# Kernel tuning notes

Hardware: AMD Instinct MI355X
Metric: run time of the kernel (lower is better)

## Reference

```python
import jax, jax.numpy as jnp
import numpy as np

N_HEAD = 16


def setup_inputs() -> dict:
    key = jax.random.key(0)
    ks = jax.random.split(key, 3)
    B, T, C = 4, 2048, 1024
    x = jax.random.normal(ks[0], (B, T, C), dtype=jnp.float32)
    w_attn = jax.random.normal(ks[1], (3 * C, C), dtype=jnp.float32) * (1.0 / np.sqrt(C))
    b_attn = jnp.zeros((3 * C,), dtype=jnp.float32)
    w_proj = jax.random.normal(ks[2], (C, C), dtype=jnp.float32) * (1.0 / np.sqrt(C))
    b_proj = jnp.zeros((C,), dtype=jnp.float32)
    return {"x": x, "w_attn": w_attn, "b_attn": b_attn, "w_proj": w_proj, "b_proj": b_proj}


def reference(x, w_attn, b_attn, w_proj, b_proj):
    B, T, C = x.shape
    H = N_HEAD
    D = C // H
    qkv = x @ w_attn.T + b_attn                      # [B, T, 3C]
    q, k, v = jnp.split(qkv, 3, axis=-1)
    # [B, T, C] -> [B, H, T, D]
    q = q.reshape(B, T, H, D).transpose(0, 2, 1, 3)
    k = k.reshape(B, T, H, D).transpose(0, 2, 1, 3)
    v = v.reshape(B, T, H, D).transpose(0, 2, 1, 3)
    scale = 1.0 / np.sqrt(D).astype(np.float32)
    att = jnp.einsum('bhqd,bhkd->bhqk', q, k) * scale  # [B, H, T, T]
    causal = jnp.tril(jnp.ones((T, T), dtype=bool))
    att = jnp.where(causal[None, None], att, -jnp.inf)
    att = jax.nn.softmax(att, axis=-1)
    y = jnp.einsum('bhqk,bhkd->bhqd', att, v)          # [B, H, T, D]
    y = y.transpose(0, 2, 1, 3).reshape(B, T, C)
    return y @ w_proj.T + b_proj
```

## Files before the change

### kernel.cpp

```cpp
#include <hip/hip_runtime.h>
#include <hip/hip_bf16.h>
#include <stdint.h>

typedef __attribute__((ext_vector_type(8))) short bf16x8;
typedef __attribute__((ext_vector_type(4))) float f32x4;

#define MFMA16(a, b, c) __builtin_amdgcn_mfma_f32_16x16x32_bf16((a), (b), (c), 0, 0, 0)

__device__ __forceinline__ unsigned short f2bf(float f) {
  unsigned int u = __builtin_bit_cast(unsigned int, f);
  unsigned int r = (u + 0x7fffu + ((u >> 16) & 1u)) >> 16;
  return (unsigned short)r;
}

__device__ __forceinline__ void gload16(const unsigned short* g, unsigned short* lds_dst) {
  __builtin_amdgcn_global_load_lds(
      (const __attribute__((address_space(1))) unsigned int*)g,
      (__attribute__((address_space(3))) unsigned int*)lds_dst, 16, 0, 0);
}

__global__ void cvt_f32_bf16(const float* __restrict__ in, unsigned short* __restrict__ out, long n) {
  long i = ((long)blockIdx.x * blockDim.x + threadIdx.x) * 4;
  long stride = (long)gridDim.x * blockDim.x * 4;
  for (; i < n; i += stride) {
    float4 v = *(const float4*)(in + i);
    ushort4 o;
    o.x = f2bf(v.x); o.y = f2bf(v.y); o.z = f2bf(v.z); o.w = f2bf(v.w);
    *(ushort4*)(out + i) = o;
  }
}

template <int EPI, int NB>
__global__ __launch_bounds__(512, 2)
void gemm_bt(const unsigned short* __restrict__ A,
             const unsigned short* __restrict__ Bt,
             const float* __restrict__ bias,
             int M, int N, int K,
             unsigned short* __restrict__ q_out,
             unsigned short* __restrict__ k_out,
             unsigned short* __restrict__ vt_out,
             float* __restrict__ f_out) {
  constexpr int BNT = NB * 64;
  alignas(16) __shared__ unsigned short Alds[2][2][128 * 64];
  alignas(16) __shared__ unsigned short Blds[2][BNT * 64];
  const int t = threadIdx.x, w = t >> 6, l = t & 63;
  const int bm = blockIdx.x, bn = blockIdx.y;
  const int wm = w >> 2, wn = w & 3;
  const int lo = l & 15, hi = l >> 4, swk = lo & 7;

  f32x4 acc[8][NB];
  const f32x4 zero = {0.f, 0.f, 0.f, 0.f};
#pragma unroll
  for (int i = 0; i < 8; ++i)
#pragma unroll
    for (int j = 0; j < NB; ++j) acc[i][j] = zero;

  const int sr = t >> 3;
  const int gsrcE = ((t & 7) ^ (sr & 7)) * 8;
  const unsigned short* Asrc = A + (long)(bm * 256 + sr) * K + gsrcE;
  const unsigned short* Bsrc = Bt + (long)(bn * BNT + sr) * K + gsrcE;

#define STAGE_AH(sb, qh, koff) do {                                    \
    unsigned short* d_ = &Alds[sb][qh][w * 512];                       \
    const unsigned short* s_ = Asrc + (long)(qh) * 64 * K + (koff);    \
    gload16(s_, d_); gload16(s_ + 128L * K, d_ + 4096); } while (0)
#define STAGE_B(sb, koff) do {                                         \
    _Pragma("unroll")                                                  \
    for (int c_ = 0; c_ < NB; ++c_)                                    \
      gload16(Bsrc + (long)c_ * 64 * K + (koff),                       \
              &Blds[sb][c_ * 4096 + w * 512]); } while (0)

  STAGE_AH(0, 0, 0);
  STAGE_B(0, 0);
  STAGE_AH(0, 1, 0);
  asm volatile("s_waitcnt vmcnt(2)" ::: "memory");
  __builtin_amdgcn_sched_barrier(0);
  __builtin_amdgcn_s_barrier();

  const int lrA = (wm * 64 + lo) * 64;
  const int lrB = (wn * (NB * 16) + lo) * 64;
  const int gk0 = ((hi) ^ swk) * 8;
  const int gk1 = ((4 + hi) ^ swk) * 8;

  bf16x8 af[4][2], blo[2][2], bhi[2];

  for (int kt = 0; kt < 16; ++kt) {
    const int c = kt & 1, nb = c ^ 1;
    const bool st = (kt < 15);
    const int koff = (kt + 1) * 64;
    const unsigned short* A0 = Alds[c][0];
    const unsigned short* A1 = Alds[c][1];
    const unsigned short* Bs = Blds[c];

#pragma unroll
    for (int ii = 0; ii < 4; ++ii) {
      af[ii][0] = *(const bf16x8*)&A0[lrA + ii * 1024 + gk0];
      af[ii][1] = *(const bf16x8*)&A0[lrA + ii * 1024 + gk1];
    }
#pragma unroll
    for (int jj = 0; jj < NB - 1; ++jj) {
      blo[jj][0] = *(const bf16x8*)&Bs[lrB + jj * 1024 + gk0];
      blo[jj][1] = *(const bf16x8*)&Bs[lrB + jj * 1024 + gk1];
    }
    if (st) STAGE_AH(nb, 0, koff);
    __builtin_amdgcn_s_barrier();
    asm volatile("s_waitcnt lgkmcnt(0)" ::: "memory");
    __builtin_amdgcn_sched_barrier(0);
    __builtin_amdgcn_s_setprio(1);
#pragma unroll
    for (int ii = 0; ii < 4; ++ii)
#pragma unroll
      for (int jj = 0; jj < NB - 1; ++jj) {
        acc[ii][jj] = MFMA16(af[ii][0], blo[jj][0], acc[ii][jj]);
        acc[ii][jj] = MFMA16(af[ii][1], blo[jj][1], acc[ii][jj]);
      }
    __builtin_amdgcn_s_setprio(0);
    __builtin_amdgcn_s_barrier();

    bhi[0] = *(const bf16x8*)&Bs[lrB + (NB - 1) * 1024 + gk0];
    bhi[1] = *(const bf16x8*)&Bs[lrB + (NB - 1) * 1024 + gk1];
    if (st) STAGE_B(nb, koff);
    __builtin_amdgcn_s_barrier();
    asm volatile("s_waitcnt lgkmcnt(0)" ::: "memory");
    __builtin_amdgcn_sched_barrier(0);
    __builtin_amdgcn_s_setprio(1);
#pragma unroll
    for (int ii = 0; ii < 4; ++ii) {
      acc[ii][NB - 1] = MFMA16(af[ii][0], bhi[0], acc[ii][NB - 1]);
      acc[ii][NB - 1] = MFMA16(af[ii][1], bhi[1], acc[ii][NB - 1]);
    }
    __builtin_amdgcn_s_setprio(0);
    if (st) {
      if constexpr (NB == 3) { asm volatile("s_waitcnt vmcnt(5)" ::: "memory"); }
      else                   { asm volatile("s_waitcnt vmcnt(4)" ::: "memory"); }
    } else {
      asm volatile("s_waitcnt vmcnt(0)" ::: "memory");
    }
    __builtin_amdgcn_sched_barrier(0);
    __builtin_amdgcn_s_barrier();

#pragma unroll
    for (int ii = 0; ii < 4; ++ii) {
      af[ii][0] = *(const bf16x8*)&A1[lrA + ii * 1024 + gk0];
      af[ii][1] = *(const bf16x8*)&A1[lrA + ii * 1024 + gk1];
    }
    if (st) STAGE_AH(nb, 1, koff);
    __builtin_amdgcn_s_barrier();
    asm volatile("s_waitcnt lgkmcnt(0)" ::: "memory");
    __builtin_amdgcn_sched_barrier(0);
    __builtin_amdgcn_s_setprio(1);
#pragma unroll
    for (int ii = 0; ii < 4; ++ii) {
      acc[4 + ii][NB - 1] = MFMA16(af[ii][0], bhi[0], acc[4 + ii][NB - 1]);
      acc[4 + ii][NB - 1] = MFMA16(af[ii][1], bhi[1], acc[4 + ii][NB - 1]);
    }
    __builtin_amdgcn_s_setprio(0);
    __builtin_amdgcn_s_barrier();

    __builtin_amdgcn_s_setprio(1);
#pragma unroll
    for (int ii = 0; ii < 4; ++ii)
#pragma unroll
      for (int jj = 0; jj < NB - 1; ++jj) {
        acc[4 + ii][jj] = MFMA16(af[ii][0], blo[jj][0], acc[4 + ii][jj]);
        acc[4 + ii][jj] = MFMA16(af[ii][1], blo[jj][1], acc[4 + ii][jj]);
      }
    __builtin_amdgcn_s_setprio(0);
    if (st) {
      asm volatile("s_waitcnt vmcnt(2)" ::: "memory");
      __builtin_amdgcn_sched_barrier(0);
    }
    __builtin_amdgcn_s_barrier();
  }
#undef STAGE_AH
#undef STAGE_B

#pragma unroll
  for (int i = 0; i < 8; ++i) {
#pragma unroll
    for (int j = 0; j < NB; ++j) {
#pragma unroll
      for (int r = 0; r < 4; ++r) {
        int row = bm * 256 + wm * 128 + i * 16 + hi * 4 + r;
        int col = bn * BNT + wn * (NB * 16) + j * 16 + lo;
        float v = acc[i][j][r] + bias[col];
        if (EPI == 0) {
          int b = row >> 11, tt = row & 2047;
          int seg = col >> 10, cc = col & 1023;
          int h = cc >> 6, d = cc & 63;
          long bh = (long)(b * 16 + h);
          if (seg == 0)      q_out[(bh * 2048 + tt) * 64 + d] = f2bf(v * 0.1803368801111f);
          else if (seg == 1) k_out[(bh * 2048 + tt) * 64 + d] = f2bf(v);
          else               vt_out[(bh * 64 + d) * 2048 + tt] = f2bf(v);
        } else {
          f_out[(long)row * N + col] = v;
        }
      }
    }
  }
}

__global__ __launch_bounds__(512, 4)
void attn_kernel(const unsigned short* __restrict__ Q,
                 const unsigned short* __restrict__ K,
                 const unsigned short* __restrict__ Vt,
                 unsigned short* __restrict__ Y) {
  alignas(16) __shared__ unsigned short Kbuf[2][64 * 64];
  alignas(16) __shared__ unsigned short Vbuf[2][64 * 64];
  alignas(16) __shared__ unsigned short pbuf[8][16 * 64];
  const int t = threadIdx.x, w = t >> 6, l = t & 63;
  const int lo = l & 15, hi = l >> 4;
  const int bh = blockIdx.x;
  const int p = blockIdx.y;
  const int b = bh >> 4, h = bh & 15;
  const int sA = p, sB = 15 - p;
  const int nA = 2 * p + 2;
  const int nTot = 34;
  const unsigned short* Qp = Q + (long)bh * 2048 * 64;
  const unsigned short* Kp = K + (long)bh * 2048 * 64;
  const unsigned short* Vp = Vt + (long)bh * 64 * 2048;
  unsigned short* pw = pbuf[w];

  const short one_bf = (short)0x3F80;
  const bf16x8 ones = {one_bf, one_bf, one_bf, one_bf, one_bf, one_bf, one_bf, one_bf};
  const f32x4 zero = {0.f, 0.f, 0.f, 0.f};

  const int qbA = sA * 128 + w * 16;
  const int qbB = sB * 128 + w * 16;

  bf16x8 qf0, qf1;
  f32x4 lsum;
  f32x4 oacc[4];

  qf0 = *(const bf16x8*)&Qp[(qbA + lo) * 64 + hi * 8];
  qf1 = *(const bf16x8*)&Qp[(qbA + lo) * 64 + 32 + hi * 8];
  lsum = zero;
#pragma unroll
  for (int dg = 0; dg < 4; ++dg) oacc[dg] = zero;

  const int srow = t >> 3;
  const int scw = ((t & 7) ^ (srow & 7)) * 8;
  const int sw = lo & 7;

#define STAGE(kvoff, bufidx)                                          \
  do {                                                                \
    unsigned short* KB_ = Kbuf[bufidx] + w * 512;                     \
    unsigned short* VB_ = Vbuf[bufidx] + w * 512;                     \
    gload16(Kp + (long)((kvoff) + srow) * 64 + scw, KB_);             \
    gload16(Vp + (long)srow * 2048 + (kvoff) + scw, VB_);             \
  } while (0)

  STAGE(0, 0);
  __syncthreads();

  for (int g = 0; g < nTot; ++g) {
    const bool inA = (g < nA);
    const int kvb = (inA ? g : g - nA) * 64;
    const int cur = g & 1;
    if (g + 1 < nTot) {
      const int jn = (g + 1 < nA) ? g + 1 : g + 1 - nA;
      STAGE(jn * 64, cur ^ 1);
    }
    const int qbase = inA ? qbA : qbB;
    if (kvb <= qbase + 15) {
      const unsigned short* KB = Kbuf[cur];
      const unsigned short* VB = Vbuf[cur];
      f32x4 s[4];
#pragma unroll
      for (int cg = 0; cg < 4; ++cg) s[cg] = zero;
      __builtin_amdgcn_s_setprio(1);
#pragma unroll
      for (int cg = 0; cg < 4; ++cg) {
        bf16x8 k0 = *(const bf16x8*)&KB[(cg * 16 + lo) * 64 + ((hi) ^ sw) * 8];
        bf16x8 k1 = *(const bf16x8*)&KB[(cg * 16 + lo) * 64 + ((4 + hi) ^ sw) * 8];
        s[cg] = MFMA16(k0, qf0, s[cg]);
        s[cg] = MFMA16(k1, qf1, s[cg]);
      }
      __builtin_amdgcn_s_setprio(0);
      if (kvb + 63 > qbase) {
        const int limit = qbase + lo - kvb;
#pragma unroll
        for (int cg = 0; cg < 4; ++cg)
#pragma unroll
          for (int r = 0; r < 4; ++r)
            if (cg * 16 + hi * 4 + r > limit) s[cg][r] = -__builtin_inff();
      }
#pragma unroll
      for (int cg = 0; cg < 4; ++cg) {
        float p0 = exp2f(s[cg][0]);
        float p1 = exp2f(s[cg][1]);
        float p2 = exp2f(s[cg][2]);
        float p3 = exp2f(s[cg][3]);
        unsigned int u0, u1;
        asm("v_cvt_pk_bf16_f32 %0, %1, %2" : "=v"(u0) : "v"(p0), "v"(p1));
        asm("v_cvt_pk_bf16_f32 %0, %1, %2" : "=v"(u1) : "v"(p2), "v"(p3));
        const int gg = (cg * 2 + (hi >> 1)) ^ sw;
        uint2 val; val.x = u0; val.y = u1;
        *(uint2*)&pw[lo * 64 + gg * 8 + (hi & 1) * 4] = val;
      }
      asm volatile("s_waitcnt lgkmcnt(0)" ::: "memory");
      bf16x8 pa0 = *(const bf16x8*)&pw[lo * 64 + ((hi) ^ sw) * 8];
      bf16x8 pa1 = *(const bf16x8*)&pw[lo * 64 + ((4 + hi) ^ sw) * 8];
      __builtin_amdgcn_s_setprio(1);
      lsum = MFMA16(pa0, ones, lsum);
      lsum = MFMA16(pa1, ones, lsum);
#pragma unroll
      for (int dg = 0; dg < 4; ++dg) {
        bf16x8 vv0 = *(const bf16x8*)&VB[(dg * 16 + lo) * 64 + ((hi) ^ sw) * 8];
        bf16x8 vv1 = *(const bf16x8*)&VB[(dg * 16 + lo) * 64 + ((4 + hi) ^ sw) * 8];
        oacc[dg] = MFMA16(pa0, vv0, oacc[dg]);
        oacc[dg] = MFMA16(pa1, vv1, oacc[dg]);
      }
      __builtin_amdgcn_s_setprio(0);
    }
    if (g == nA - 1) {
#pragma unroll
      for (int r = 0; r < 4; ++r) {
        float inv = 1.0f / lsum[r];
        int rowg = qbA + hi * 4 + r;
        long base = ((long)b * 2048 + rowg) * 1024 + h * 64;
#pragma unroll
        for (int dg = 0; dg < 4; ++dg)
          Y[base + dg * 16 + lo] = f2bf(oacc[dg][r] * inv);
      }
      qf0 = *(const bf16x8*)&Qp[(qbB + lo) * 64 + hi * 8];
      qf1 = *(const bf16x8*)&Qp[(qbB + lo) * 64 + 32 + hi * 8];
      lsum = zero;
#pragma unroll
      for (int dg = 0; dg < 4; ++dg) oacc[dg] = zero;
    }
    __syncthreads();
  }

#pragma unroll
  for (int r = 0; r < 4; ++r) {
    float inv = 1.0f / lsum[r];
    int rowg = qbB + hi * 4 + r;
    long base = ((long)b * 2048 + rowg) * 1024 + h * 64;
#pragma unroll
    for (int dg = 0; dg < 4; ++dg)
      Y[base + dg * 16 + lo] = f2bf(oacc[dg][r] * inv);
  }
#undef STAGE
}

extern "C" void kernel_launch(void* const* d_in, const int* in_sizes, int n_in,
                              void* d_out, int out_size, void* d_ws, size_t ws_size,
                              hipStream_t stream) {
  const float* x      = (const float*)d_in[0];
  const float* w_attn = (const float*)d_in[1];
  const float* b_attn = (const float*)d_in[2];
  const float* w_proj = (const float*)d_in[3];
  const float* b_proj = (const float*)d_in[4];
  float* out = (float*)d_out;

  const long NX = 8192L * 1024;
  const long NWA = 3072L * 1024;
  const long NWP = 1024L * 1024;
  const long NQ = 64L * 2048 * 64;

  char* ws = (char*)d_ws;
  unsigned short* xb  = (unsigned short*)ws; ws += NX * 2;
  unsigned short* wab = (unsigned short*)ws; ws += NWA * 2;
  unsigned short* wpb = (unsigned short*)ws; ws += NWP * 2;
  unsigned short* qb  = (unsigned short*)ws; ws += NQ * 2;
  unsigned short* kb  = (unsigned short*)ws; ws += NQ * 2;
  unsigned short* vtb = (unsigned short*)ws; ws += NQ * 2;
  unsigned short* yb  = (unsigned short*)ws; ws += NX * 2;

  cvt_f32_bf16<<<2048, 256, 0, stream>>>(x, xb, NX);
  cvt_f32_bf16<<<768, 256, 0, stream>>>(w_attn, wab, NWA);
  cvt_f32_bf16<<<256, 256, 0, stream>>>(w_proj, wpb, NWP);

  dim3 g1(32, 16);
  gemm_bt<0, 3><<<g1, 512, 0, stream>>>(xb, wab, b_attn, 8192, 3072, 1024,
                                        qb, kb, vtb, nullptr);
  dim3 ga(64, 8);
  attn_kernel<<<ga, 512, 0, stream>>>(qb, kb, vtb, yb);
  dim3 g2(32, 8);
  gemm_bt<1, 2><<<g2, 512, 0, stream>>>(yb, wpb, b_proj, 8192, 1024, 1024,
                                        nullptr, nullptr, nullptr, out);
}
```

Before: 180.7 us.

## Process 32 query rows per wave in attention to reuse K/V fragments

Each attention wave now handles two 16-row query sub-tiles (32 rows), so every K and V fragment read from LDS feeds twice as many MFMAs. Each block covers 256-row query tiles, paired causally as before, and the grid drops from 512 to 256 blocks. The launch-bounds occupancy target is lowered to 2 and the P staging buffer is doubled. The aim is to cut LDS reads and global K/V staging per unit of work, at the cost of higher register pressure and fewer blocks, which could leave the 256 CUs underfilled.

```diff
diff --git a/kernel.cpp b/kernel.cpp
--- a/kernel.cpp
+++ b/kernel.cpp
@@ -200,22 +200,22 @@
   }
 }
 
-__global__ __launch_bounds__(512, 4)
+__global__ __launch_bounds__(512, 2)
 void attn_kernel(const unsigned short* __restrict__ Q,
                  const unsigned short* __restrict__ K,
                  const unsigned short* __restrict__ Vt,
                  unsigned short* __restrict__ Y) {
   alignas(16) __shared__ unsigned short Kbuf[2][64 * 64];
   alignas(16) __shared__ unsigned short Vbuf[2][64 * 64];
-  alignas(16) __shared__ unsigned short pbuf[8][16 * 64];
+  alignas(16) __shared__ unsigned short pbuf[8][32 * 64];
   const int t = threadIdx.x, w = t >> 6, l = t & 63;
   const int lo = l & 15, hi = l >> 4;
   const int bh = blockIdx.x;
   const int p = blockIdx.y;
   const int b = bh >> 4, h = bh & 15;
-  const int sA = p, sB = 15 - p;
-  const int nA = 2 * p + 2;
-  const int nTot = 34;
+  const int sA = p, sB = 7 - p;
+  const int nA = 4 * p + 4;
+  const int nTot = 36;
   const unsigned short* Qp = Q + (long)bh * 2048 * 64;
   const unsigned short* Kp = K + (long)bh * 2048 * 64;
   const unsigned short* Vp = Vt + (long)bh * 64 * 2048;
@@ -225,18 +225,20 @@
   const bf16x8 ones = {one_bf, one_bf, one_bf, one_bf, one_bf, one_bf, one_bf, one_bf};
   const f32x4 zero = {0.f, 0.f, 0.f, 0.f};
 
-  const int qbA = sA * 128 + w * 16;
-  const int qbB = sB * 128 + w * 16;
-
-  bf16x8 qf0, qf1;
-  f32x4 lsum;
-  f32x4 oacc[4];
-
-  qf0 = *(const bf16x8*)&Qp[(qbA + lo) * 64 + hi * 8];
-  qf1 = *(const bf16x8*)&Qp[(qbA + lo) * 64 + 32 + hi * 8];
-  lsum = zero;
-#pragma unroll
-  for (int dg = 0; dg < 4; ++dg) oacc[dg] = zero;
+  const int qbA = sA * 256 + w * 32;
+  const int qbB = sB * 256 + w * 32;
+
+  bf16x8 qa0, qa1, qb0, qb1;
+  f32x4 lsA, lsB;
+  f32x4 oaccA[4], oaccB[4];
+
+  qa0 = *(const bf16x8*)&Qp[(qbA + lo) * 64 + hi * 8];
+  qa1 = *(const bf16x8*)&Qp[(qbA + lo) * 64 + 32 + hi * 8];
+  qb0 = *(const bf16x8*)&Qp[(qbA + 16 + lo) * 64 + hi * 8];
+  qb1 = *(const bf16x8*)&Qp[(qbA + 16 + lo) * 64 + 32 + hi * 8];
+  lsA = zero; lsB = zero;
+#pragma unroll
+  for (int dg = 0; dg < 4; ++dg) { oaccA[dg] = zero; oaccB[dg] = zero; }
 
   const int srow = t >> 3;
   const int scw = ((t & 7) ^ (srow & 7)) * 8;
@@ -262,84 +264,119 @@
       STAGE(jn * 64, cur ^ 1);
     }
     const int qbase = inA ? qbA : qbB;
-    if (kvb <= qbase + 15) {
+    if (kvb <= qbase + 31) {
       const unsigned short* KB = Kbuf[cur];
       const unsigned short* VB = Vbuf[cur];
-      f32x4 s[4];
-#pragma unroll
-      for (int cg = 0; cg < 4; ++cg) s[cg] = zero;
+      f32x4 sa[4], sb[4];
+#pragma unroll
+      for (int cg = 0; cg < 4; ++cg) { sa[cg] = zero; sb[cg] = zero; }
       __builtin_amdgcn_s_setprio(1);
 #pragma unroll
       for (int cg = 0; cg < 4; ++cg) {
         bf16x8 k0 = *(const bf16x8*)&KB[(cg * 16 + lo) * 64 + ((hi) ^ sw) * 8];
         bf16x8 k1 = *(const bf16x8*)&KB[(cg * 16 + lo) * 64 + ((4 + hi) ^ sw) * 8];
-        s[cg] = MFMA16(k0, qf0, s[cg]);
-        s[cg] = MFMA16(k1, qf1, s[cg]);
+        sa[cg] = MFMA16(k0, qa0, sa[cg]);
+        sa[cg] = MFMA16(k1, qa1, sa[cg]);
+        sb[cg] = MFMA16(k0, qb0, sb[cg]);
+        sb[cg] = MFMA16(k1, qb1, sb[cg]);
       }
       __builtin_amdgcn_s_setprio(0);
       if (kvb + 63 > qbase) {
-        const int limit = qbase + lo - kvb;
+        const int la = qbase + lo - kvb;
+        const int lb = la + 16;
 #pragma unroll
         for (int cg = 0; cg < 4; ++cg)
 #pragma unroll
-          for (int r = 0; r < 4; ++r)
-            if (cg * 16 + hi * 4 + r > limit) s[cg][r] = -__builtin_inff();
+          for (int r = 0; r < 4; ++r) {
+            const int ki = cg * 16 + hi * 4 + r;
+            if (ki > la) sa[cg][r] = -__builtin_inff();
+            if (ki > lb) sb[cg][r] = -__builtin_inff();
+          }
       }
 #pragma unroll
       for (int cg = 0; cg < 4; ++cg) {
-        float p0 = exp2f(s[cg][0]);
-        float p1 = exp2f(s[cg][1]);
-        float p2 = exp2f(s[cg][2]);
-        float p3 = exp2f(s[cg][3]);
-        unsigned int u0, u1;
-        asm("v_cvt_pk_bf16_f32 %0, %1, %2" : "=v"(u0) : "v"(p0), "v"(p1));
-        asm("v_cvt_pk_bf16_f32 %0, %1, %2" : "=v"(u1) : "v"(p2), "v"(p3));
         const int gg = (cg * 2 + (hi >> 1)) ^ sw;
-        uint2 val; val.x = u0; val.y = u1;
-        *(uint2*)&pw[lo * 64 + gg * 8 + (hi & 1) * 4] = val;
+        {
+          float p0 = exp2f(sa[cg][0]);
+          float p1 = exp2f(sa[cg][1]);
+          float p2 = exp2f(sa[cg][2]);
+          float p3 = exp2f(sa[cg][3]);
+          unsigned int u0, u1;
+          asm("v_cvt_pk_bf16_f32 %0, %1, %2" : "=v"(u0) : "v"(p0), "v"(p1));
+          asm("v_cvt_pk_bf16_f32 %0, %1, %2" : "=v"(u1) : "v"(p2), "v"(p3));
+          uint2 val; val.x = u0; val.y = u1;
+          *(uint2*)&pw[lo * 64 + gg * 8 + (hi & 1) * 4] = val;
+        }
+        {
+          float p0 = exp2f(sb[cg][0]);
+          float p1 = exp2f(sb[cg][1]);
+          float p2 = exp2f(sb[cg][2]);
+          float p3 = exp2f(sb[cg][3]);
+          unsigned int u0, u1;
+          asm("v_cvt_pk_bf16_f32 %0, %1, %2" : "=v"(u0) : "v"(p0), "v"(p1));
+          asm("v_cvt_pk_bf16_f32 %0, %1, %2" : "=v"(u1) : "v"(p2), "v"(p3));
+          uint2 val; val.x = u0; val.y = u1;
+          *(uint2*)&pw[(16 + lo) * 64 + gg * 8 + (hi & 1) * 4] = val;
+        }
       }
       asm volatile("s_waitcnt lgkmcnt(0)" ::: "memory");
-      bf16x8 pa0 = *(const bf16x8*)&pw[lo * 64 + ((hi) ^ sw) * 8];
-      bf16x8 pa1 = *(const bf16x8*)&pw[lo * 64 + ((4 + hi) ^ sw) * 8];
+      bf16x8 pA0 = *(const bf16x8*)&pw[lo * 64 + ((hi) ^ sw) * 8];
+      bf16x8 pA1 = *(const bf16x8*)&pw[lo * 64 + ((4 + hi) ^ sw) * 8];
+      bf16x8 pB0 = *(const bf16x8*)&pw[(16 + lo) * 64 + ((hi) ^ sw) * 8];
+      bf16x8 pB1 = *(const bf16x8*)&pw[(16 + lo) * 64 + ((4 + hi) ^ sw) * 8];
       __builtin_amdgcn_s_setprio(1);
-      lsum = MFMA16(pa0, ones, lsum);
-      lsum = MFMA16(pa1, ones, lsum);
+      lsA = MFMA16(pA0, ones, lsA);
+      lsA = MFMA16(pA1, ones, lsA);
+      lsB = MFMA16(pB0, ones, lsB);
+      lsB = MFMA16(pB1, ones, lsB);
 #pragma unroll
       for (int dg = 0; dg < 4; ++dg) {
         bf16x8 vv0 = *(const bf16x8*)&VB[(dg * 16 + lo) * 64 + ((hi) ^ sw) * 8];
         bf16x8 vv1 = *(const bf16x8*)&VB[(dg * 16 + lo) * 64 + ((4 + hi) ^ sw) * 8];
-        oacc[dg] = MFMA16(pa0, vv0, oacc[dg]);
-        oacc[dg] = MFMA16(pa1, vv1, oacc[dg]);
+        oaccA[dg] = MFMA16(pA0, vv0, oaccA[dg]);
+        oaccA[dg] = MFMA16(pA1, vv1, oaccA[dg]);
+        oaccB[dg] = MFMA16(pB0, vv0, oaccB[dg]);
+        oaccB[dg] = MFMA16(pB1, vv1, oaccB[dg]);
       }
       __builtin_amdgcn_s_setprio(0);
     }
     if (g == nA - 1) {
 #pragma unroll
       for (int r = 0; r < 4; ++r) {
-        float inv = 1.0f / lsum[r];
-        int rowg = qbA + hi * 4 + r;
-        long base = ((long)b * 2048 + rowg) * 1024 + h * 64;
-#pragma unroll
-        for (int dg = 0; dg < 4; ++dg)
-          Y[base + dg * 16 + lo] = f2bf(oacc[dg][r] * inv);
-      }
-      qf0 = *(const bf16x8*)&Qp[(qbB + lo) * 64 + hi * 8];
-      qf1 = *(const bf16x8*)&Qp[(qbB + lo) * 64 + 32 + hi * 8];
-      lsum = zero;
-#pragma unroll
-      for (int dg = 0; dg < 4; ++dg) oacc[dg] = zero;
+        float invA = 1.0f / lsA[r];
+        float invB = 1.0f / lsB[r];
+        int rowgA = qbA + hi * 4 + r;
+        long baseA = ((long)b * 2048 + rowgA) * 1024 + h * 64;
+        long baseB = baseA + 16 * 1024;
+#pragma unroll
+        for (int dg = 0; dg < 4; ++dg) {
+          Y[baseA + dg * 16 + lo] = f2bf(oaccA[dg][r] * invA);
+          Y[baseB + dg * 16 + lo] = f2bf(oaccB[dg][r] * invB);
+        }
+      }
+      qa0 = *(const bf16x8*)&Qp[(qbB + lo) * 64 + hi * 8];
+      qa1 = *(const bf16x8*)&Qp[(qbB + lo) * 64 + 32 + hi * 8];
+      qb0 = *(const bf16x8*)&Qp[(qbB + 16 + lo) * 64 + hi * 8];
+      qb1 = *(const bf16x8*)&Qp[(qbB + 16 + lo) * 64 + 32 + hi * 8];
+      lsA = zero; lsB = zero;
+#pragma unroll
+      for (int dg = 0; dg < 4; ++dg) { oaccA[dg] = zero; oaccB[dg] = zero; }
     }
     __syncthreads();
   }
 
 #pragma unroll
   for (int r = 0; r < 4; ++r) {
-    float inv = 1.0f / lsum[r];
-    int rowg = qbB + hi * 4 + r;
-    long base = ((long)b * 2048 + rowg) * 1024 + h * 64;
-#pragma unroll
-    for (int dg = 0; dg < 4; ++dg)
-      Y[base + dg * 16 + lo] = f2bf(oacc[dg][r] * inv);
+    float invA = 1.0f / lsA[r];
+    float invB = 1.0f / lsB[r];
+    int rowgA = qbB + hi * 4 + r;
+    long baseA = ((long)b * 2048 + rowgA) * 1024 + h * 64;
+    long baseB = baseA + 16 * 1024;
+#pragma unroll
+    for (int dg = 0; dg < 4; ++dg) {
+      Y[baseA + dg * 16 + lo] = f2bf(oaccA[dg][r] * invA);
+      Y[baseB + dg * 16 + lo] = f2bf(oaccB[dg][r] * invB);
+    }
   }
 #undef STAGE
 }
@@ -375,7 +412,7 @@
   dim3 g1(32, 16);
   gemm_bt<0, 3><<<g1, 512, 0, stream>>>(xb, wab, b_attn, 8192, 3072, 1024,
                                         qb, kb, vtb, nullptr);
-  dim3 ga(64, 8);
+  dim3 ga(64, 4);
   attn_kernel<<<ga, 512, 0, stream>>>(qb, kb, vtb, yb);
   dim3 g2(32, 8);
   gemm_bt<1, 2><<<g2, 512, 0, stream>>>(yb, wpb, b_proj, 8192, 1024, 1024,
```

After: 184.6 us. 2.2% more time.
